# Kernel optimization log

Measured on AMD Instinct MI355X. Metric: run time of the kernel, lower is better.

The kernel has to match this reference:

```python
import jax, jax.numpy as jnp
import numpy as np

EMBED_DIM = 1024
NUM_HEADS = 16
HEAD_DIM = EMBED_DIM // NUM_HEADS


def setup_inputs() -> dict:
    key = jax.random.key(0)
    ks = jax.random.split(key, 9)
    B, L, D = 4, 2048, EMBED_DIM
    s = 1.0 / np.sqrt(D)
    return {
        "inputs": jax.random.normal(ks[0], (B, L, D), dtype=jnp.float32),
        "wq": jax.random.normal(ks[1], (D, D), dtype=jnp.float32) * s,
        "bq": jax.random.normal(ks[2], (D,), dtype=jnp.float32) * s,
        "wk": jax.random.normal(ks[3], (D, D), dtype=jnp.float32) * s,
        "bk": jax.random.normal(ks[4], (D,), dtype=jnp.float32) * s,
        "wv": jax.random.normal(ks[5], (D, D), dtype=jnp.float32) * s,
        "bv": jax.random.normal(ks[6], (D,), dtype=jnp.float32) * s,
        "wo": jax.random.normal(ks[7], (D, D), dtype=jnp.float32) * s,
        "bo": jax.random.normal(ks[8], (D,), dtype=jnp.float32) * s,
    }


def reference(inputs, wq, bq, wk, bk, wv, bv, wo, bo):
    B, L, D = inputs.shape
    H, Hd = NUM_HEADS, HEAD_DIM
    # Linear projections (torch Linear: x @ W^T + b)
    q = inputs @ wq.T + bq
    k = inputs @ wk.T + bk
    v = inputs @ wv.T + bv
    # (B, L, D) -> (B, H, L, Hd)
    q = q.reshape(B, L, H, Hd).transpose(0, 2, 1, 3)
    k = k.reshape(B, L, H, Hd).transpose(0, 2, 1, 3)
    v = v.reshape(B, L, H, Hd).transpose(0, 2, 1, 3)
    scale = 1.0 / np.sqrt(Hd).astype(np.float32)
    scores = jnp.einsum("bhqd,bhkd->bhqk", q, k) * scale  # (B,H,L,L)
    attn = jax.nn.softmax(scores, axis=-1)
    out = jnp.einsum("bhqk,bhkd->bhqd", attn, v)  # (B,H,L,Hd)
    out = out.transpose(0, 2, 1, 3).reshape(B, L, D)
    return out @ wo.T + bo
```

## Files before the change

### kernel.cpp

```cpp
#include <hip/hip_runtime.h>

typedef __attribute__((ext_vector_type(8))) short short8;
typedef __attribute__((ext_vector_type(8))) unsigned short ushort8;
typedef __attribute__((ext_vector_type(4))) unsigned short ushort4_t;
typedef __attribute__((ext_vector_type(4))) unsigned u32x4;
typedef __attribute__((ext_vector_type(4))) float f32x4;
typedef __attribute__((ext_vector_type(16))) float f32x16;

#define GLOAD_LDS(gp, lp) \
  __builtin_amdgcn_global_load_lds((const __attribute__((address_space(1))) void*)(gp), \
                                   (__attribute__((address_space(3))) void*)(lp), 16, 0, 0)

static __device__ __forceinline__ unsigned short f2bf(float f) {
  unsigned int u = __float_as_uint(f);
  u = u + 0x7fffu + ((u >> 16) & 1u);
  return (unsigned short)(u >> 16);
}

static __device__ __forceinline__ float exp2i(float x) {
  float r;
  asm("v_exp_f32 %0, %1" : "=v"(r) : "v"(x));
  return r;
}

static __device__ __forceinline__ unsigned cvtpk(float a, float b) {
  unsigned r;
  asm("v_cvt_pk_bf16_f32 %0, %1, %2" : "=v"(r) : "v"(a), "v"(b));
  return r;
}

static __device__ __forceinline__ void pl32swap(unsigned& a, unsigned& b) {
  asm("v_permlane32_swap_b32 %0, %1" : "+v"(a), "+v"(b));
}

__global__ __launch_bounds__(256) void cvt_bf16(const float* __restrict__ in,
                                                unsigned short* __restrict__ out,
                                                int n) {
  int i = (blockIdx.x * 256 + threadIdx.x) * 8;
  if (i >= n) return;
  const float4* p = reinterpret_cast<const float4*>(in + i);
  float4 a = p[0], b = p[1];
  ushort8 o;
  o[0] = f2bf(a.x); o[1] = f2bf(a.y); o[2] = f2bf(a.z); o[3] = f2bf(a.w);
  o[4] = f2bf(b.x); o[5] = f2bf(b.y); o[6] = f2bf(b.z); o[7] = f2bf(b.w);
  *reinterpret_cast<ushort8*>(out + i) = o;
}

__global__ __launch_bounds__(256) void cvt_w4(const float* __restrict__ i0, const float* __restrict__ i1,
                                              const float* __restrict__ i2, const float* __restrict__ i3,
                                              unsigned short* __restrict__ o0, unsigned short* __restrict__ o1,
                                              unsigned short* __restrict__ o2, unsigned short* __restrict__ o3) {
  int w = blockIdx.y;
  const float* in = (w == 0) ? i0 : (w == 1) ? i1 : (w == 2) ? i2 : i3;
  unsigned short* out = (w == 0) ? o0 : (w == 1) ? o1 : (w == 2) ? o2 : o3;
  int i = (blockIdx.x * 256 + threadIdx.x) * 8;
  const float4* p = reinterpret_cast<const float4*>(in + i);
  float4 a = p[0], b = p[1];
  ushort8 o;
  o[0] = f2bf(a.x); o[1] = f2bf(a.y); o[2] = f2bf(a.z); o[3] = f2bf(a.w);
  o[4] = f2bf(b.x); o[5] = f2bf(b.y); o[6] = f2bf(b.z); o[7] = f2bf(b.w);
  *reinterpret_cast<ushort8*>(out + i) = o;
}

template <int MODE>
__global__ __launch_bounds__(256) void gemm_bt(const unsigned short* __restrict__ A,
                                               const unsigned short* __restrict__ B,
                                               const float* __restrict__ bias,
                                               void* __restrict__ Cptr,
                                               int M, int N, int K, float scale) {
  __shared__ char As[2][16384];
  __shared__ char Bs[2][16384];
  const int t = threadIdx.x;
  const int lane = t & 63, wave = t >> 6;
  const int wm = wave >> 1, wn = wave & 1;
  const int m0 = blockIdx.y * 128, n0 = blockIdx.x * 128;

  const unsigned short* aS[4];
  const unsigned short* bS[4];
#pragma unroll
  for (int j = 0; j < 4; j++) {
    int i = wave * 256 + j * 64 + lane;
    int r = i >> 3, c = ((i & 7) ^ (r & 7)) << 3;
    aS[j] = A + (size_t)(m0 + r) * K + c;
    bS[j] = B + (size_t)(n0 + r) * K + c;
  }

  f32x4 acc[4][4] = {};
  const int NT = K >> 6;

#pragma unroll
  for (int j = 0; j < 4; j++) {
    GLOAD_LDS(aS[j], As[0] + wave * 4096 + j * 1024);
    GLOAD_LDS(bS[j], Bs[0] + wave * 4096 + j * 1024);
  }

  for (int kt = 0; kt < NT; kt++) {
    const int cur = kt & 1;
    __syncthreads();
    if (kt + 1 < NT) {
      int ko = (kt + 1) << 6;
#pragma unroll
      for (int j = 0; j < 4; j++) {
        GLOAD_LDS(aS[j] + ko, As[cur ^ 1] + wave * 4096 + j * 1024);
        GLOAD_LDS(bS[j] + ko, Bs[cur ^ 1] + wave * 4096 + j * 1024);
      }
    }
    const char* Ac = As[cur];
    const char* Bc = Bs[cur];
#pragma unroll
    for (int ks = 0; ks < 2; ks++) {
      short8 af[4], bfr[4];
#pragma unroll
      for (int x = 0; x < 4; x++) {
        int arow = wm * 64 + x * 16 + (lane & 15);
        int kk = ks * 32 + (lane >> 4) * 8;
        af[x] = *reinterpret_cast<const short8*>(Ac + (((arow * 64 + kk) * 2) ^ ((arow & 7) << 4)));
        int brow = wn * 64 + x * 16 + (lane & 15);
        bfr[x] = *reinterpret_cast<const short8*>(Bc + (((brow * 64 + kk) * 2) ^ ((brow & 7) << 4)));
      }
      __builtin_amdgcn_s_setprio(1);
#pragma unroll
      for (int mi = 0; mi < 4; mi++)
#pragma unroll
        for (int ni = 0; ni < 4; ni++)
          acc[mi][ni] = __builtin_amdgcn_mfma_f32_16x16x32_bf16(af[mi], bfr[ni], acc[mi][ni], 0, 0, 0);
      __builtin_amdgcn_s_setprio(0);
    }
  }

#pragma unroll
  for (int mi = 0; mi < 4; mi++) {
#pragma unroll
    for (int ni = 0; ni < 4; ni++) {
      int n = n0 + wn * 64 + ni * 16 + (lane & 15);
      float bs = bias[n];
      int mbase = m0 + wm * 64 + mi * 16 + ((lane >> 4) << 2);
      if (MODE == 2) {
        int b = mbase >> 11, l = mbase & 2047;
        ushort4_t o;
#pragma unroll
        for (int r = 0; r < 4; r++) o[r] = f2bf(acc[mi][ni][r] + bs);
        *reinterpret_cast<ushort4_t*>((unsigned short*)Cptr + (size_t)(b * N + n) * 2048 + l) = o;
      } else if (MODE == 0) {
#pragma unroll
        for (int r = 0; r < 4; r++)
          ((unsigned short*)Cptr)[(size_t)(mbase + r) * N + n] = f2bf((acc[mi][ni][r] + bs) * scale);
      } else {
#pragma unroll
        for (int r = 0; r < 4; r++)
          ((float*)Cptr)[(size_t)(mbase + r) * N + n] = acc[mi][ni][r] + bs;
      }
    }
  }
}

__global__ __launch_bounds__(256) void attn_fwd(const unsigned short* __restrict__ Q,
                                                const unsigned short* __restrict__ Kb,
                                                const unsigned short* __restrict__ Vt,
                                                unsigned short* __restrict__ O) {
  const int h = blockIdx.y;
  const int b = blockIdx.z;
  const int q0 = blockIdx.x * 128;
  __shared__ char Ks[2][8192];
  __shared__ char Vs[2][8192];
  const int t = threadIdx.x, lane = t & 63, wave = t >> 6;
  const int ql = lane & 31;
  const int hi = lane >> 5;
  const int qrow = q0 + wave * 32 + ql;
  const int sw = (ql & 7) << 4;

  int lo_[4];
#pragma unroll
  for (int st = 0; st < 4; st++) lo_[st] = (ql * 128 + sw) ^ (st * 32 + hi * 16);

  const int ic0 = wave * 128 + lane, ic1 = ic0 + 64;
  const int r0 = ic0 >> 3, c0 = ((ic0 & 7) ^ (r0 & 7)) << 3;
  const int r1 = ic1 >> 3, c1 = ((ic1 & 7) ^ (r1 & 7)) << 3;
  const unsigned short* kS0 = Kb + (size_t)(b * 2048 + r0) * 1024 + h * 64 + c0;
  const unsigned short* kS1 = Kb + (size_t)(b * 2048 + r1) * 1024 + h * 64 + c1;
  const unsigned short* vS0 = Vt + ((size_t)(b * 16 + h) * 64 + r0) * 2048 + c0;
  const unsigned short* vS1 = Vt + ((size_t)(b * 16 + h) * 64 + r1) * 2048 + c1;

  short8 qf[4];
  {
    const unsigned short* qp = Q + (size_t)(b * 2048 + qrow) * 1024 + h * 64 + hi * 8;
#pragma unroll
    for (int st = 0; st < 4; st++) qf[st] = *reinterpret_cast<const short8*>(qp + st * 16);
  }

  const short one_bf = (short)0x3F80;
  const short8 ones = {one_bf, one_bf, one_bf, one_bf, one_bf, one_bf, one_bf, one_bf};

  f32x16 accd0 = {}, accd1 = {};
  f32x16 accl = {};

  GLOAD_LDS(kS0, Ks[0] + wave * 2048);
  GLOAD_LDS(kS1, Ks[0] + wave * 2048 + 1024);
  GLOAD_LDS(vS0, Vs[0] + wave * 2048);
  GLOAD_LDS(vS1, Vs[0] + wave * 2048 + 1024);

#pragma unroll 2
  for (int kt = 0; kt < 32; kt++) {
    const int cur = kt & 1;
    __syncthreads();
    if (kt + 1 < 32) {
      size_t ko = (size_t)(kt + 1) * 65536;
      int vo = (kt + 1) * 64;
      GLOAD_LDS(kS0 + ko, Ks[cur ^ 1] + wave * 2048);
      GLOAD_LDS(kS1 + ko, Ks[cur ^ 1] + wave * 2048 + 1024);
      GLOAD_LDS(vS0 + vo, Vs[cur ^ 1] + wave * 2048);
      GLOAD_LDS(vS1 + vo, Vs[cur ^ 1] + wave * 2048 + 1024);
    }
    const char* Kc = Ks[cur];
    const char* Vc = Vs[cur];

    f32x16 s0 = {}, s1 = {};
    __builtin_amdgcn_s_setprio(1);
#pragma unroll
    for (int st = 0; st < 4; st++) {
      short8 k0 = *reinterpret_cast<const short8*>(Kc + lo_[st]);
      short8 k1 = *reinterpret_cast<const short8*>(Kc + lo_[st] + 4096);
      s0 = __builtin_amdgcn_mfma_f32_32x32x16_bf16(k0, qf[st], s0, 0, 0, 0);
      s1 = __builtin_amdgcn_mfma_f32_32x32x16_bf16(k1, qf[st], s1, 0, 0, 0);
    }
    __builtin_amdgcn_s_setprio(0);

#pragma unroll
    for (int r = 0; r < 16; r++) s0[r] = exp2i(s0[r]);
#pragma unroll
    for (int r = 0; r < 16; r++) s1[r] = exp2i(s1[r]);

    short8 pf0, pf1, pf2, pf3;
    {
      unsigned w0 = cvtpk(s0[0], s0[1]), w1 = cvtpk(s0[2], s0[3]);
      unsigned w2 = cvtpk(s0[4], s0[5]), w3 = cvtpk(s0[6], s0[7]);
      pl32swap(w0, w2); pl32swap(w1, w3);
      u32x4 p0 = {w0, w1, w2, w3};
      pf0 = __builtin_bit_cast(short8, p0);
      unsigned w4 = cvtpk(s0[8], s0[9]), w5 = cvtpk(s0[10], s0[11]);
      unsigned w6 = cvtpk(s0[12], s0[13]), w7 = cvtpk(s0[14], s0[15]);
      pl32swap(w4, w6); pl32swap(w5, w7);
      u32x4 p1 = {w4, w5, w6, w7};
      pf1 = __builtin_bit_cast(short8, p1);
      unsigned x0 = cvtpk(s1[0], s1[1]), x1 = cvtpk(s1[2], s1[3]);
      unsigned x2 = cvtpk(s1[4], s1[5]), x3 = cvtpk(s1[6], s1[7]);
      pl32swap(x0, x2); pl32swap(x1, x3);
      u32x4 p2 = {x0, x1, x2, x3};
      pf2 = __builtin_bit_cast(short8, p2);
      unsigned x4 = cvtpk(s1[8], s1[9]), x5 = cvtpk(s1[10], s1[11]);
      unsigned x6 = cvtpk(s1[12], s1[13]), x7 = cvtpk(s1[14], s1[15]);
      pl32swap(x4, x6); pl32swap(x5, x7);
      u32x4 p3 = {x4, x5, x6, x7};
      pf3 = __builtin_bit_cast(short8, p3);
    }

    __builtin_amdgcn_s_setprio(1);
#pragma unroll
    for (int st = 0; st < 4; st++) {
      short8 pb = (st == 0) ? pf0 : (st == 1) ? pf1 : (st == 2) ? pf2 : pf3;
      short8 v0 = *reinterpret_cast<const short8*>(Vc + lo_[st]);
      short8 v1 = *reinterpret_cast<const short8*>(Vc + lo_[st] + 4096);
      accd0 = __builtin_amdgcn_mfma_f32_32x32x16_bf16(v0, pb, accd0, 0, 0, 0);
      accd1 = __builtin_amdgcn_mfma_f32_32x32x16_bf16(v1, pb, accd1, 0, 0, 0);
      accl  = __builtin_amdgcn_mfma_f32_32x32x16_bf16(ones, pb, accl, 0, 0, 0);
    }
    __builtin_amdgcn_s_setprio(0);
  }

  float inv = 1.0f / accl[0];
  unsigned short* op = O + (size_t)(b * 2048 + qrow) * 1024 + h * 64;
#pragma unroll
  for (int g = 0; g < 4; g++) {
    ushort4_t o0, o1;
#pragma unroll
    for (int j = 0; j < 4; j++) {
      o0[j] = f2bf(accd0[4 * g + j] * inv);
      o1[j] = f2bf(accd1[4 * g + j] * inv);
    }
    *reinterpret_cast<ushort4_t*>(op + 8 * g + 4 * hi) = o0;
    *reinterpret_cast<ushort4_t*>(op + 32 + 8 * g + 4 * hi) = o1;
  }
}

extern "C" void kernel_launch(void* const* d_in, const int* in_sizes, int n_in,
                              void* d_out, int out_size, void* d_ws, size_t ws_size,
                              hipStream_t stream) {
  const float* X = (const float*)d_in[0];
  const float* wq = (const float*)d_in[1];
  const float* bq = (const float*)d_in[2];
  const float* wk = (const float*)d_in[3];
  const float* bk = (const float*)d_in[4];
  const float* wv = (const float*)d_in[5];
  const float* bv = (const float*)d_in[6];
  const float* wo = (const float*)d_in[7];
  const float* bo = (const float*)d_in[8];

  char* ws = (char*)d_ws;
  const size_t MB = 1024 * 1024;
  unsigned short* Xb  = (unsigned short*)(ws + 0);
  unsigned short* Wqb = (unsigned short*)(ws + 16 * MB);
  unsigned short* Wkb = (unsigned short*)(ws + 18 * MB);
  unsigned short* Wvb = (unsigned short*)(ws + 20 * MB);
  unsigned short* Wob = (unsigned short*)(ws + 22 * MB);
  unsigned short* Qb  = (unsigned short*)(ws + 24 * MB);
  unsigned short* Kb  = (unsigned short*)(ws + 40 * MB);
  unsigned short* Vtb = (unsigned short*)(ws + 56 * MB);
  unsigned short* Ob  = (unsigned short*)(ws + 72 * MB);

  cvt_bf16<<<8388608 / 2048, 256, 0, stream>>>(X, Xb, 8388608);
  cvt_w4<<<dim3(512, 4), 256, 0, stream>>>(wq, wk, wv, wo, Wqb, Wkb, Wvb, Wob);

  const float QSCALE = 0.125f * 1.4426950408889634f;
  dim3 gg(8, 64);
  gemm_bt<0><<<gg, 256, 0, stream>>>(Xb, Wqb, bq, Qb, 8192, 1024, 1024, QSCALE);
  gemm_bt<0><<<gg, 256, 0, stream>>>(Xb, Wkb, bk, Kb, 8192, 1024, 1024, 1.0f);
  gemm_bt<2><<<gg, 256, 0, stream>>>(Xb, Wvb, bv, Vtb, 8192, 1024, 1024, 1.0f);

  attn_fwd<<<dim3(16, 16, 4), 256, 0, stream>>>(Qb, Kb, Vtb, Ob);

  gemm_bt<1><<<gg, 256, 0, stream>>>(Ob, Wob, bo, (float*)d_out, 8192, 1024, 1024, 1.0f);
}
```

Measured before the change: 213.8 us.

## Replace ones-MFMA row sum with VALU sums, merge conversion kernels, set occupancy

The attention kernel no longer spends a third MFMA per step multiplying by a ones matrix to get the softmax denominator. Instead it sums the exponentiated scores in f32 registers and combines the two half-waves with a shuffle at the end. The input and weight bf16 conversion kernels are merged into one launch. attn_fwd also gets a min-blocks-per-CU hint of 4. This cuts matrix-core work, one launch and an accumulator register tile, at the cost of extra VALU adds. The denominator now sums unrounded f32 values rather than the bf16-rounded ones fed to the PV product.

```diff
diff --git a/kernel.cpp b/kernel.cpp
--- a/kernel.cpp
+++ b/kernel.cpp
@@ -33,27 +33,25 @@
   asm("v_permlane32_swap_b32 %0, %1" : "+v"(a), "+v"(b));
 }
 
-__global__ __launch_bounds__(256) void cvt_bf16(const float* __restrict__ in,
-                                                unsigned short* __restrict__ out,
-                                                int n) {
-  int i = (blockIdx.x * 256 + threadIdx.x) * 8;
-  if (i >= n) return;
-  const float4* p = reinterpret_cast<const float4*>(in + i);
-  float4 a = p[0], b = p[1];
-  ushort8 o;
-  o[0] = f2bf(a.x); o[1] = f2bf(a.y); o[2] = f2bf(a.z); o[3] = f2bf(a.w);
-  o[4] = f2bf(b.x); o[5] = f2bf(b.y); o[6] = f2bf(b.z); o[7] = f2bf(b.w);
-  *reinterpret_cast<ushort8*>(out + i) = o;
-}
-
-__global__ __launch_bounds__(256) void cvt_w4(const float* __restrict__ i0, const float* __restrict__ i1,
-                                              const float* __restrict__ i2, const float* __restrict__ i3,
-                                              unsigned short* __restrict__ o0, unsigned short* __restrict__ o1,
-                                              unsigned short* __restrict__ o2, unsigned short* __restrict__ o3) {
-  int w = blockIdx.y;
-  const float* in = (w == 0) ? i0 : (w == 1) ? i1 : (w == 2) ? i2 : i3;
-  unsigned short* out = (w == 0) ? o0 : (w == 1) ? o1 : (w == 2) ? o2 : o3;
-  int i = (blockIdx.x * 256 + threadIdx.x) * 8;
+__global__ __launch_bounds__(256) void cvt_all(const float* __restrict__ X,
+                                               const float* __restrict__ w0, const float* __restrict__ w1,
+                                               const float* __restrict__ w2, const float* __restrict__ w3,
+                                               unsigned short* __restrict__ Xb,
+                                               unsigned short* __restrict__ o0, unsigned short* __restrict__ o1,
+                                               unsigned short* __restrict__ o2, unsigned short* __restrict__ o3) {
+  int bid = blockIdx.x;
+  const float* in;
+  unsigned short* out;
+  int i;
+  if (bid < 4096) {
+    in = X; out = Xb; i = bid * 2048 + threadIdx.x * 8;
+  } else {
+    int idx = bid - 4096;
+    int w = idx >> 9;
+    in = (w == 0) ? w0 : (w == 1) ? w1 : (w == 2) ? w2 : w3;
+    out = (w == 0) ? o0 : (w == 1) ? o1 : (w == 2) ? o2 : o3;
+    i = (idx & 511) * 2048 + threadIdx.x * 8;
+  }
   const float4* p = reinterpret_cast<const float4*>(in + i);
   float4 a = p[0], b = p[1];
   ushort8 o;
@@ -154,10 +152,10 @@
   }
 }
 
-__global__ __launch_bounds__(256) void attn_fwd(const unsigned short* __restrict__ Q,
-                                                const unsigned short* __restrict__ Kb,
-                                                const unsigned short* __restrict__ Vt,
-                                                unsigned short* __restrict__ O) {
+__global__ __launch_bounds__(256, 4) void attn_fwd(const unsigned short* __restrict__ Q,
+                                                   const unsigned short* __restrict__ Kb,
+                                                   const unsigned short* __restrict__ Vt,
+                                                   unsigned short* __restrict__ O) {
   const int h = blockIdx.y;
   const int b = blockIdx.z;
   const int q0 = blockIdx.x * 128;
@@ -188,11 +186,8 @@
     for (int st = 0; st < 4; st++) qf[st] = *reinterpret_cast<const short8*>(qp + st * 16);
   }
 
-  const short one_bf = (short)0x3F80;
-  const short8 ones = {one_bf, one_bf, one_bf, one_bf, one_bf, one_bf, one_bf, one_bf};
-
+  float l_run = 0.f;
   f32x16 accd0 = {}, accd1 = {};
-  f32x16 accl = {};
 
   GLOAD_LDS(kS0, Ks[0] + wave * 2048);
   GLOAD_LDS(kS1, Ks[0] + wave * 2048 + 1024);
@@ -225,13 +220,16 @@
     }
     __builtin_amdgcn_s_setprio(0);
 
-#pragma unroll
-    for (int r = 0; r < 16; r++) s0[r] = exp2i(s0[r]);
-#pragma unroll
-    for (int r = 0; r < 16; r++) s1[r] = exp2i(s1[r]);
-
     short8 pf0, pf1, pf2, pf3;
+    float rs;
     {
+#pragma unroll
+      for (int r = 0; r < 16; r++) s0[r] = exp2i(s0[r]);
+      float a0 = (s0[0] + s0[1]) + (s0[2] + s0[3]);
+      float a1 = (s0[4] + s0[5]) + (s0[6] + s0[7]);
+      float a2 = (s0[8] + s0[9]) + (s0[10] + s0[11]);
+      float a3 = (s0[12] + s0[13]) + (s0[14] + s0[15]);
+      rs = (a0 + a1) + (a2 + a3);
       unsigned w0 = cvtpk(s0[0], s0[1]), w1 = cvtpk(s0[2], s0[3]);
       unsigned w2 = cvtpk(s0[4], s0[5]), w3 = cvtpk(s0[6], s0[7]);
       pl32swap(w0, w2); pl32swap(w1, w3);
@@ -242,6 +240,15 @@
       pl32swap(w4, w6); pl32swap(w5, w7);
       u32x4 p1 = {w4, w5, w6, w7};
       pf1 = __builtin_bit_cast(short8, p1);
+    }
+    {
+#pragma unroll
+      for (int r = 0; r < 16; r++) s1[r] = exp2i(s1[r]);
+      float a0 = (s1[0] + s1[1]) + (s1[2] + s1[3]);
+      float a1 = (s1[4] + s1[5]) + (s1[6] + s1[7]);
+      float a2 = (s1[8] + s1[9]) + (s1[10] + s1[11]);
+      float a3 = (s1[12] + s1[13]) + (s1[14] + s1[15]);
+      rs += (a0 + a1) + (a2 + a3);
       unsigned x0 = cvtpk(s1[0], s1[1]), x1 = cvtpk(s1[2], s1[3]);
       unsigned x2 = cvtpk(s1[4], s1[5]), x3 = cvtpk(s1[6], s1[7]);
       pl32swap(x0, x2); pl32swap(x1, x3);
@@ -253,6 +260,7 @@
       u32x4 p3 = {x4, x5, x6, x7};
       pf3 = __builtin_bit_cast(short8, p3);
     }
+    l_run += rs;
 
     __builtin_amdgcn_s_setprio(1);
 #pragma unroll
@@ -262,12 +270,12 @@
       short8 v1 = *reinterpret_cast<const short8*>(Vc + lo_[st] + 4096);
       accd0 = __builtin_amdgcn_mfma_f32_32x32x16_bf16(v0, pb, accd0, 0, 0, 0);
       accd1 = __builtin_amdgcn_mfma_f32_32x32x16_bf16(v1, pb, accd1, 0, 0, 0);
-      accl  = __builtin_amdgcn_mfma_f32_32x32x16_bf16(ones, pb, accl, 0, 0, 0);
     }
     __builtin_amdgcn_s_setprio(0);
   }
 
-  float inv = 1.0f / accl[0];
+  float l_tot = l_run + __shfl_xor(l_run, 32);
+  float inv = 1.0f / l_tot;
   unsigned short* op = O + (size_t)(b * 2048 + qrow) * 1024 + h * 64;
 #pragma unroll
   for (int g = 0; g < 4; g++) {
@@ -307,8 +315,7 @@
   unsigned short* Vtb = (unsigned short*)(ws + 56 * MB);
   unsigned short* Ob  = (unsigned short*)(ws + 72 * MB);
 
-  cvt_bf16<<<8388608 / 2048, 256, 0, stream>>>(X, Xb, 8388608);
-  cvt_w4<<<dim3(512, 4), 256, 0, stream>>>(wq, wk, wv, wo, Wqb, Wkb, Wvb, Wob);
+  cvt_all<<<4096 + 4 * 512, 256, 0, stream>>>(X, wq, wk, wv, wo, Xb, Wqb, Wkb, Wvb, Wob);
 
   const float QSCALE = 0.125f * 1.4426950408889634f;
   dim3 gg(8, 64);
```

Result: faster. 197.7 us (-7.5%).
